# Kernel tuning notes

Hardware: AMD Instinct MI355X
Metric: run time of the kernel (lower is better)

## Reference

```python
import jax, jax.numpy as jnp
import numpy as np

UNITS = 1024
IN_DIM = 1024
B, T = 32, 2048


def setup_inputs() -> dict:
    key = jax.random.key(0)
    k1, k2, k3 = jax.random.split(key, 3)
    # glorot-uniform style scaling for weights
    lim_k = float(np.sqrt(6.0 / (IN_DIM + UNITS)))
    lim_r = float(np.sqrt(6.0 / (UNITS + UNITS)))
    x = jax.random.normal(k1, (B, T, IN_DIM), dtype=jnp.float32)
    kernel = jax.random.uniform(k2, (IN_DIM, UNITS), minval=-lim_k, maxval=lim_k, dtype=jnp.float32)
    recurrent_kernel = jax.random.uniform(k3, (UNITS, UNITS), minval=-lim_r, maxval=lim_r, dtype=jnp.float32)
    h0 = jnp.zeros((B, UNITS), dtype=jnp.float32)
    return {"x": x, "h0": h0, "kernel": kernel, "recurrent_kernel": recurrent_kernel}


def reference(x, h0, kernel, recurrent_kernel):
    # MinimalRNNCell: h_t = x_t @ W_in + h_{t-1} @ W_rec (purely linear, no activation)
    # Hoist the input projection out of the scan: one big GEMM over [B*T, IN_DIM].
    xin = jnp.einsum('btd,du->btu', x, kernel)  # [B, T, U]

    def step(h, xt):
        h_new = xt + h @ recurrent_kernel
        return h_new, None

    # scan over time axis; Keras RNN default returns the last output [B, U]
    h_last, _ = jax.lax.scan(step, h0, jnp.swapaxes(xin, 0, 1))
    return h_last
```

## Files before the change

kernel.cpp:

```cpp
#include <hip/hip_runtime.h>
#include <cstddef>
#include <cstdint>


namespace {

constexpr int BATCH = 32;
constexpr int T = 2048;
constexpr int U = 1024;
constexpr int LJ = 8;
constexpr int CJ = T / LJ;
constexpr int MJ = CJ * BATCH;

typedef _Float16 f16;
typedef _Float16 f16x4 __attribute__((ext_vector_type(4)));
typedef _Float16 f16x8 __attribute__((ext_vector_type(8)));
typedef float f32x4 __attribute__((ext_vector_type(4)));

__device__ inline void gload16(const void* g, void* l) {
    __builtin_amdgcn_global_load_lds(
        (const __attribute__((address_space(1))) unsigned int*)g,
        (__attribute__((address_space(3))) unsigned int*)l, 16, 0, 0);
}

__global__ __launch_bounds__(256)
void split_x(const float* __restrict__ x, f16* __restrict__ xh, long n4)
{
    long i = (long)blockIdx.x * 256 + threadIdx.x;
    const long stride = (long)gridDim.x * 256;
    for (; i < n4; i += stride) {
        const float4 v = *(const float4*)(x + i * 4);
        f16x4 h;
        h.x = (f16)v.x; h.y = (f16)v.y; h.z = (f16)v.z; h.w = (f16)v.w;
        *(f16x4*)(xh + i * 4) = h;
    }
}

__global__ __launch_bounds__(256)
void tsplit2(const float* __restrict__ S0, f16* __restrict__ Dh0, f16* __restrict__ Dl0,
             long dstride0, long doff0,
             const float* __restrict__ S1, f16* __restrict__ Dh1, f16* __restrict__ Dl1,
             long dstride1, long doff1)
{
    const float* S = blockIdx.z ? S1 : S0;
    f16* Dh = blockIdx.z ? Dh1 : Dh0;
    f16* Dl = blockIdx.z ? Dl1 : Dl0;
    const long dstride = blockIdx.z ? dstride1 : dstride0;
    const long doff = blockIdx.z ? doff1 : doff0;

    __shared__ float tile[32][33];
    const int t = threadIdx.x;
    const int k0 = blockIdx.x * 32;
    const int n0 = blockIdx.y * 32;
    {
        const int r = t >> 3, c4 = (t & 7) << 2;
        const float4 v = *(const float4*)(S + (size_t)(k0 + r) * U + n0 + c4);
        tile[r][c4 + 0] = v.x; tile[r][c4 + 1] = v.y;
        tile[r][c4 + 2] = v.z; tile[r][c4 + 3] = v.w;
    }
    __syncthreads();
    {
        const int c = t >> 3, r4 = (t & 7) << 2;
        float v0 = tile[r4 + 0][c], v1 = tile[r4 + 1][c],
              v2 = tile[r4 + 2][c], v3 = tile[r4 + 3][c];
        f16x4 h, lo;
        h.x = (f16)v0; lo.x = (f16)((v0 - (float)h.x) * 2048.0f);
        h.y = (f16)v1; lo.y = (f16)((v1 - (float)h.y) * 2048.0f);
        h.z = (f16)v2; lo.z = (f16)((v2 - (float)h.z) * 2048.0f);
        h.w = (f16)v3; lo.w = (f16)((v3 - (float)h.w) * 2048.0f);
        const size_t o = (size_t)(n0 + c) * dstride + doff + k0 + r4;
        *(f16x4*)(Dh + o) = h;
        *(f16x4*)(Dl + o) = lo;
    }
}

__global__ __launch_bounds__(512, 2)
void main4(const f16* __restrict__ xh, const f16* __restrict__ GhT,
           const f16* __restrict__ GlT, float* __restrict__ g0)
{
    __shared__ __align__(16) f16 LA[2][16384];
    __shared__ __align__(16) f16 LBh[2][8192];
    __shared__ __align__(16) f16 LBl[2][8192];

    const int tid  = threadIdx.x;
    const int lane = tid & 63;
    const int w    = tid >> 6;
    const int wm   = w >> 1;
    const int wn   = w & 1;
    const int r0   = blockIdx.x * 256;
    const int c0   = blockIdx.y * 128;

    const int ch  = tid & 7;
    const int rid = tid >> 3;

    size_t aof[4];
    #pragma unroll
    for (int q = 0; q < 4; ++q) {
        const int m = q * 64 + rid;
        const int arow = r0 + m;
        const size_t xbase = ((size_t)(arow & 31) * T + (size_t)(arow >> 5) * LJ) * U;
        aof[q] = xbase * 2 + (size_t)((ch ^ (m & 7)) << 4);
    }
    size_t bof[2];
    #pragma unroll
    for (int q = 0; q < 2; ++q) {
        const int c = q * 64 + rid;
        bof[q] = ((size_t)(c0 + c) << 14) + (size_t)((ch ^ (c & 7)) << 4);
    }
    const int dst = tid << 4;

    f32x4 hh[4][4], xx[4][4];
    #pragma unroll
    for (int mi = 0; mi < 4; ++mi)
        #pragma unroll
        for (int ni = 0; ni < 4; ++ni) {
            hh[mi][ni] = (f32x4){0.f, 0.f, 0.f, 0.f};
            xx[mi][ni] = (f32x4){0.f, 0.f, 0.f, 0.f};
        }

    auto stage = [&](int b, int kt) {
        const size_t kb = (size_t)kt << 7;
        #pragma unroll
        for (int q = 0; q < 4; ++q)
            gload16((const char*)xh + aof[q] + kb, (char*)&LA[b][0] + q * 8192 + dst);
        #pragma unroll
        for (int q = 0; q < 2; ++q) {
            gload16((const char*)GhT + bof[q] + kb, (char*)&LBh[b][0] + q * 8192 + dst);
            gload16((const char*)GlT + bof[q] + kb, (char*)&LBl[b][0] + q * 8192 + dst);
        }
    };

    stage(0, 0);
    __syncthreads();

    int buf = 0;
    #pragma unroll 1
    for (int kt = 0; kt < 128; ++kt) {
        if (kt + 1 < 128) stage(buf ^ 1, kt + 1);

        #pragma unroll
        for (int ks = 0; ks < 2; ++ks) {
            const int kg = ks * 4 + (lane >> 4);
            f16x8 af[4], bh[4], bl[4];
            #pragma unroll
            for (int mi = 0; mi < 4; ++mi) {
                const int rr = wm * 64 + mi * 16 + (lane & 15);
                const int byte = rr * 128 + ((kg ^ (rr & 7)) << 4);
                af[mi] = *(const f16x8*)((const char*)&LA[buf][0] + byte);
            }
            #pragma unroll
            for (int ni = 0; ni < 4; ++ni) {
                const int cc = wn * 64 + ni * 16 + (lane & 15);
                const int byte = cc * 128 + ((kg ^ (cc & 7)) << 4);
                bh[ni] = *(const f16x8*)((const char*)&LBh[buf][0] + byte);
                bl[ni] = *(const f16x8*)((const char*)&LBl[buf][0] + byte);
            }
            #pragma unroll
            for (int mi = 0; mi < 4; ++mi)
                #pragma unroll
                for (int ni = 0; ni < 4; ++ni) {
                    hh[mi][ni] = __builtin_amdgcn_mfma_f32_16x16x32_f16(af[mi], bh[ni], hh[mi][ni], 0, 0, 0);
                    xx[mi][ni] = __builtin_amdgcn_mfma_f32_16x16x32_f16(af[mi], bl[ni], xx[mi][ni], 0, 0, 0);
                }
        }
        __syncthreads();
        buf ^= 1;
    }

    #pragma unroll
    for (int mi = 0; mi < 4; ++mi)
        #pragma unroll
        for (int ni = 0; ni < 4; ++ni) {
            const int col = c0 + wn * 64 + ni * 16 + (lane & 15);
            #pragma unroll
            for (int r = 0; r < 4; ++r) {
                const int row = r0 + wm * 64 + mi * 16 + ((lane >> 4) << 2) + r;
                g0[(size_t)row * U + col] = hh[mi][ni][r] + xx[mi][ni][r] * (1.0f / 2048.0f);
            }
        }
}

struct MDesc {
    const float* A;
    const f16* BhT; const f16* BlT;
    float* C;
    f16* EhT; f16* ElT;
    long bstride, estride, eoff;
    int M, K;
    int amode;
    int cmode;
    float ascale, cscale, escale;
};

__global__ __launch_bounds__(256, 2)
void mk(MDesc d0, MDesc d1)
{
    MDesc d = blockIdx.z ? d1 : d0;
    const int r0 = blockIdx.y * 128;
    if (r0 >= d.M) return;
    const int c0 = blockIdx.x * 64;

    __shared__ __align__(16) f16 SMEM[24576];
    f16 (*LAs)[2][4096] = (f16(*)[2][4096])(&SMEM[0]);
    f16 (*LBs)[2][2048] = (f16(*)[2][2048])(&SMEM[16384]);

    const int tid = threadIdx.x;
    const int lane = tid & 63;
    const int w = tid >> 6;
    const int wm = w >> 1, wn = w & 1;

    const int arr = tid >> 1;
    const int ahalf = tid & 1;
    int arow = r0 + arr;
    if (arow >= d.M) arow = d.M - 1;
    const float* aP;
    if (d.amode == 2)
        aP = d.A + ((size_t)(((arow >> 5) << 6) + (arow & 31)) << 10);
    else
        aP = d.A + (size_t)arow * d.K;
    aP += ahalf * 16;
    int awb[2];
    #pragma unroll
    for (int j = 0; j < 2; ++j) {
        const int prow = arr >> 1;
        const int chn = 4 * (arr & 1) + 2 * ahalf + j;
        awb[j] = prow * 128 + ((chn ^ (prow & 7)) << 4);
    }

    const int bprow = tid >> 3;
    const int bslot = tid & 7;
    const int bchn  = bslot ^ (bprow & 7);
    const size_t bsrc = (size_t)(c0 + 2 * bprow + (bchn >> 2)) * (size_t)d.bstride * 2
                      + (size_t)((bchn & 3) << 4);
    const int bdst = tid * 16;

    f32x4 hh[4][2], xx[4][2];
    #pragma unroll
    for (int mi = 0; mi < 4; ++mi)
        #pragma unroll
        for (int ni = 0; ni < 2; ++ni) {
            hh[mi][ni] = (f32x4){0.f, 0.f, 0.f, 0.f};
            xx[mi][ni] = (f32x4){0.f, 0.f, 0.f, 0.f};
        }

    float4 areg[4];
    auto aload = [&](int kt) {
        const float* ap = aP + (size_t)kt * 32;
        #pragma unroll
        for (int i = 0; i < 4; ++i) areg[i] = *(const float4*)(ap + i * 4);
    };
    auto awrite = [&](int b) {
        #pragma unroll
        for (int j = 0; j < 2; ++j) {
            f16x8 h8, l8;
            #pragma unroll
            for (int e = 0; e < 2; ++e) {
                float4 v = areg[j * 2 + e];
                v.x *= d.ascale; v.y *= d.ascale; v.z *= d.ascale; v.w *= d.ascale;
                #pragma unroll
                for (int t2 = 0; t2 < 4; ++t2) {
                    const float f = (&v.x)[t2];
                    const f16 hv = (f16)f;
                    h8[e * 4 + t2] = hv;
                    l8[e * 4 + t2] = (f16)((f - (float)hv) * 2048.0f);
                }
            }
            *(f16x8*)((char*)&LAs[b][0][0] + awb[j]) = h8;
            *(f16x8*)((char*)&LAs[b][1][0] + awb[j]) = l8;
        }
    };
    auto bload = [&](int b, int kt) {
        const size_t kb = (size_t)kt << 6;
        gload16((const char*)d.BhT + bsrc + kb, (char*)&LBs[b][0][0] + bdst);
        gload16((const char*)d.BlT + bsrc + kb, (char*)&LBs[b][1][0] + bdst);
    };

    aload(0); bload(0, 0); awrite(0);
    __syncthreads();

    const int NT = d.K >> 5;
    int buf = 0;
    #pragma unroll 1
    for (int kt = 0; kt < NT; ++kt) {
        const bool more = (kt + 1 < NT);
        if (more) { aload(kt + 1); bload(buf ^ 1, kt + 1); }

        {
            const int kg = lane >> 4;
            f16x8 ah[4], al[4], bh[2], bl[2];
            #pragma unroll
            for (int mi = 0; mi < 4; ++mi) {
                const int rr = wm * 64 + mi * 16 + (lane & 15);
                const int prow = rr >> 1;
                const int chn = 4 * (rr & 1) + kg;
                const int byte = prow * 128 + ((chn ^ (prow & 7)) << 4);
                ah[mi] = *(const f16x8*)((const char*)&LAs[buf][0][0] + byte);
                al[mi] = *(const f16x8*)((const char*)&LAs[buf][1][0] + byte);
            }
            #pragma unroll
            for (int ni = 0; ni < 2; ++ni) {
                const int cc = wn * 32 + ni * 16 + (lane & 15);
                const int prow = cc >> 1;
                const int chn = 4 * (cc & 1) + kg;
                const int byte = prow * 128 + ((chn ^ (prow & 7)) << 4);
                bh[ni] = *(const f16x8*)((const char*)&LBs[buf][0][0] + byte);
                bl[ni] = *(const f16x8*)((const char*)&LBs[buf][1][0] + byte);
            }
            #pragma unroll
            for (int mi = 0; mi < 4; ++mi)
                #pragma unroll
                for (int ni = 0; ni < 2; ++ni) {
                    hh[mi][ni] = __builtin_amdgcn_mfma_f32_16x16x32_f16(ah[mi], bh[ni], hh[mi][ni], 0, 0, 0);
                    xx[mi][ni] = __builtin_amdgcn_mfma_f32_16x16x32_f16(ah[mi], bl[ni], xx[mi][ni], 0, 0, 0);
                    xx[mi][ni] = __builtin_amdgcn_mfma_f32_16x16x32_f16(al[mi], bh[ni], xx[mi][ni], 0, 0, 0);
                }
        }

        if (more) awrite(buf ^ 1);
        __syncthreads();
        buf ^= 1;
    }

    const bool emit = (d.EhT != nullptr);
    f16* Ehs = &SMEM[0];
    f16* Els = &SMEM[8192];

    #pragma unroll
    for (int mi = 0; mi < 4; ++mi) {
        #pragma unroll
        for (int ni = 0; ni < 2; ++ni) {
            const int orow = wm * 64 + mi * 16 + ((lane >> 4) << 2);
            const int colL = wn * 32 + ni * 16 + (lane & 15);
            const int col  = c0 + colL;
            float v[4];
            #pragma unroll
            for (int r = 0; r < 4; ++r)
                v[r] = (hh[mi][ni][r] + xx[mi][ni][r] * (1.0f / 2048.0f)) * d.cscale;
            if (d.C) {
                #pragma unroll
                for (int r = 0; r < 4; ++r) {
                    const int grow = r0 + orow + r;
                    if (grow < d.M) {
                        float o = v[r];
                        if (d.amode == 2) {
                            const int arow2 = (((grow >> 5) << 6) + (grow & 31)) + 32;
                            o += d.A[(size_t)arow2 * U + col];
                        }
                        float* cp = d.C + (size_t)grow * U + col;
                        if (d.cmode == 1) *cp += o; else *cp = o;
                    }
                }
            }
            if (emit) {
                f16x4 h4, l4;
                #pragma unroll
                for (int r = 0; r < 4; ++r) {
                    const float e = v[r] * d.escale;
                    h4[r] = (f16)e;
                    l4[r] = (f16)((e - (float)h4[r]) * 2048.0f);
                }
                const int blk = orow >> 3;
                const int boff = colL * 256 + ((blk ^ (colL & 15)) << 4) + (orow & 7) * 2;
                *(f16x4*)((char*)Ehs + boff) = h4;
                *(f16x4*)((char*)Els + boff) = l4;
            }
        }
    }

    if (emit) {
        __syncthreads();
        const int c  = tid & 63;
        const int b0 = (tid >> 6) * 4;
        const size_t gbase = (size_t)(c0 + c) * d.estride + d.eoff + (size_t)r0;
        #pragma unroll
        for (int i = 0; i < 4; ++i) {
            const int blk = b0 + i;
            const int off = c * 256 + ((blk ^ (c & 15)) << 4);
            *(f16x8*)(d.EhT + gbase + blk * 8) = *(const f16x8*)((char*)Ehs + off);
            *(f16x8*)(d.ElT + gbase + blk * 8) = *(const f16x8*)((char*)Els + off);
        }
    }
}

}

extern "C" void kernel_launch(void* const* d_in, const int* in_sizes, int n_in,
                              void* d_out, int out_size, void* d_ws, size_t ws_size,
                              hipStream_t stream) {
    const float* x  = (const float*)d_in[0];
    const float* h0 = (const float*)d_in[1];
    const float* W  = (const float*)d_in[2];
    const float* R  = (const float*)d_in[3];
    float* out = (float*)d_out;

    const size_t UU = (size_t)U * U;
    float* Gf  = (float*)d_ws;
    float* g0  = Gf + 4 * UU;
    float* g1  = g0 + (size_t)MJ * U;
    float* Rp2 = g1 + (size_t)(MJ / 2) * U;
    float* Rp4 = Rp2 + UU;
    float* Qa  = Rp4 + UU;
    float* Qb  = Qa + UU;
    f16* GhT = (f16*)(Qb + UU);
    f16* GlT = GhT + (size_t)U * 8192;
    f16* Tb  = GlT + (size_t)U * 8192;
    f16* Th[5]; f16* Tl[5];
    for (int i = 0; i < 5; ++i) { Th[i] = Tb + (size_t)i * 2 * UU; Tl[i] = Th[i] + UU; }
    f16* xh = Tb + 10 * UU;

    auto MD = [](const float* A, const f16* Bh, const f16* Bl, float* C,
                 f16* Eh, f16* El, long eoff, long estride, long bstride,
                 int M, int K, int amode, int cmode,
                 float as_, float cs_, float es_) {
        MDesc d;
        d.A = A; d.BhT = Bh; d.BlT = Bl; d.C = C; d.EhT = Eh; d.ElT = El;
        d.bstride = bstride; d.estride = estride; d.eoff = eoff;
        d.M = M; d.K = K; d.amode = amode; d.cmode = cmode;
        d.ascale = as_; d.cscale = cs_; d.escale = es_;
        return d;
    };
    MDesc dz = MD(nullptr, nullptr, nullptr, nullptr, nullptr, nullptr,
                  0, 0, 1024, 0, 64, 0, 0, 1.f, 1.f, 1.f);
    auto MKpair = [&](MDesc a, MDesc b) {
        int y0 = (a.M + 127) >> 7, y1 = (b.M + 127) >> 7;
        int y = y0 > y1 ? y0 : y1; if (y < 1) y = 1;
        mk<<<dim3(U / 64, (unsigned)y, 2), 256, 0, stream>>>(a, b);
    };

    split_x<<<2048, 256, 0, stream>>>(x, xh, (long)BATCH * T * U / 4);
    tsplit2<<<dim3(32, 32, 2), 256, 0, stream>>>(R, Th[0], Tl[0], 1024, 0,
                                                 W, GhT, GlT, 8192, 7 * 1024);
    hipMemcpyAsync(Gf + 3 * UU, W, UU * sizeof(float), hipMemcpyDeviceToDevice, stream);

    MKpair(MD(R,   Th[0], Tl[0], Rp2,        Th[1], Tl[1], 0,    1024, 1024, U,     U, 0, 0, 1.f, 1.f, 1.f),
           MD(W,   Th[0], Tl[0], Gf + 2*UU,  GhT,   GlT,   6144, 8192, 1024, U,     U, 0, 0, 1.f, 1.f, 1.f));
    MKpair(MD(Rp2, Th[1], Tl[1], Rp4,        Th[2], Tl[2], 0,    1024, 1024, U,     U, 0, 0, 1.f, 1.f, 1.f),
           MD(Gf + 2*UU, Th[1], Tl[1], Gf,   GhT,   GlT,   4096, 8192, 1024, 2 * U, U, 0, 0, 1.f, 1.f, 1.f));
    MKpair(MD(Rp4, Th[2], Tl[2], Qa,         Th[3], Tl[3], 0,    1024, 1024, U,     U, 0, 0, 1.f, 1.f, 1.f),
           MD(Gf,  Th[2], Tl[2], nullptr,    GhT,   GlT,   0,    8192, 1024, 4 * U, U, 0, 0, 1.f, 1.f, 1.f));

    main4<<<dim3(32, 8), 512, 0, stream>>>(xh, GhT, GlT, g0);

    MKpair(MD(h0, Th[3], Tl[3], g0, nullptr, nullptr, 0, 0, 1024, BATCH, U, 0, 1, 1.f, 1.f, 1.f), dz);

    const float aS[8] = {1.f, 1.f, 1.f, 1.f, 1.f,
                         1.f / 64.f, 1.f / 1048576.f, 7.105427357601002e-15f};
    const float cS[8] = {1.f, 1.f, 1.f, 1.f, 1.f,
                         64.f, 68719476736.f , 1.5474250491067253e26f };
    float* Qcur = Qa; float* Qnxt = Qb;
    int tcur = 3, tnxt = 4;
    float* cur = g0; float* nxt = g1;
    for (int l = 0; l < 8; ++l) {
        const int M = BATCH * ((CJ / 2) >> l);
        MDesc dc = MD(cur, Th[tcur], Tl[tcur], (l == 7) ? out : nxt,
                      nullptr, nullptr, 0, 0, 1024, M, U, 2, 0, aS[l], cS[l], 1.f);
        MDesc dq = dz;
        if (l < 7) {
            float sq_as = 1.f, sq_cs = 1.f, sq_es = 1.f;
            float* sqC = Qnxt;
            if (l == 5) { sq_es = 1.0f / 65536.0f; }
            if (l == 6) { sq_as = 1.0f / 16777216.0f; sqC = nullptr; }
            dq = MD(Qcur, Th[tcur], Tl[tcur], sqC, Th[tnxt], Tl[tnxt],
                    0, 1024, 1024, U, U, 0, 0, sq_as, sq_cs, sq_es);
        }
        MKpair(dc, dq);
        float* tq = Qcur; Qcur = Qnxt; Qnxt = tq;
        int ts = tcur; tcur = tnxt; tnxt = ts;
        float* tg = cur; cur = nxt; nxt = tg;
    }
    (void)in_sizes; (void)n_in; (void)out_size; (void)ws_size;
}
```

Before: 839.2 us.

## Pre-split GEMM A operands into fp16 hi/lo and stage via direct LDS loads

Producers now write the fp16 hi/lo split of their fp32 outputs into separate row-major buffers, alongside the transposed split they already wrote. Consumer GEMMs can then load the A operand with global_load_lds, as B already is, instead of reading fp32, scaling and splitting in registers and writing LDS. The scan schedule is also restructured: the Q-power chain is shifted one step ahead, with the first Q step paired with the h0 correction, and a third g buffer is rotated. This removes per-tile conversion ALU work and register staging from the GEMM main loop. In exchange, producers issue extra scattered fp16 stores, and the workspace holds many more split copies.

```diff
diff --git a/kernel.cpp b/kernel.cpp
--- a/kernel.cpp
+++ b/kernel.cpp
@@ -37,16 +37,22 @@
 }
 
 __global__ __launch_bounds__(256)
-void tsplit2(const float* __restrict__ S0, f16* __restrict__ Dh0, f16* __restrict__ Dl0,
-             long dstride0, long doff0,
-             const float* __restrict__ S1, f16* __restrict__ Dh1, f16* __restrict__ Dl1,
-             long dstride1, long doff1)
+void prep(const float* __restrict__ R, const float* __restrict__ W,
+          const float* __restrict__ h0,
+          f16* __restrict__ TTRh, f16* __restrict__ TTRl,
+          f16* __restrict__ Rrh, f16* __restrict__ Rrl,
+          f16* __restrict__ GhT, f16* __restrict__ GlT,
+          f16* __restrict__ Wrh, f16* __restrict__ Wrl,
+          f16* __restrict__ h0rh, f16* __restrict__ h0rl)
 {
-    const float* S = blockIdx.z ? S1 : S0;
-    f16* Dh = blockIdx.z ? Dh1 : Dh0;
-    f16* Dl = blockIdx.z ? Dl1 : Dl0;
-    const long dstride = blockIdx.z ? dstride1 : dstride0;
-    const long doff = blockIdx.z ? doff1 : doff0;
+    const int z = blockIdx.z;
+    const float* S = z ? W : R;
+    f16* Dh = z ? GhT : TTRh;
+    f16* Dl = z ? GlT : TTRl;
+    const long dstride = z ? 8192 : 1024;
+    const long doff = z ? 7168 : 0;
+    f16* Rh_ = z ? Wrh : Rrh;
+    f16* Rl_ = z ? Wrl : Rrl;
 
     __shared__ float tile[32][33];
     const int t = threadIdx.x;
@@ -57,6 +63,14 @@
         const float4 v = *(const float4*)(S + (size_t)(k0 + r) * U + n0 + c4);
         tile[r][c4 + 0] = v.x; tile[r][c4 + 1] = v.y;
         tile[r][c4 + 2] = v.z; tile[r][c4 + 3] = v.w;
+        f16x4 h, lo;
+        h.x = (f16)v.x; lo.x = (f16)((v.x - (float)h.x) * 2048.0f);
+        h.y = (f16)v.y; lo.y = (f16)((v.y - (float)h.y) * 2048.0f);
+        h.z = (f16)v.z; lo.z = (f16)((v.z - (float)h.z) * 2048.0f);
+        h.w = (f16)v.w; lo.w = (f16)((v.w - (float)h.w) * 2048.0f);
+        const size_t ro = (size_t)(k0 + r) * U + n0 + c4;
+        *(f16x4*)(Rh_ + ro) = h;
+        *(f16x4*)(Rl_ + ro) = lo;
     }
     __syncthreads();
     {
@@ -72,11 +86,24 @@
         *(f16x4*)(Dh + o) = h;
         *(f16x4*)(Dl + o) = lo;
     }
+    if (z == 1 && blockIdx.x == 0) {
+        const int r = t >> 3, c4 = (t & 7) << 2;
+        const float4 v = *(const float4*)(h0 + (size_t)r * U + n0 + c4);
+        f16x4 h, lo;
+        h.x = (f16)v.x; lo.x = (f16)((v.x - (float)h.x) * 2048.0f);
+        h.y = (f16)v.y; lo.y = (f16)((v.y - (float)h.y) * 2048.0f);
+        h.z = (f16)v.z; lo.z = (f16)((v.z - (float)h.z) * 2048.0f);
+        h.w = (f16)v.w; lo.w = (f16)((v.w - (float)h.w) * 2048.0f);
+        const size_t ro = (size_t)r * U + n0 + c4;
+        *(f16x4*)(h0rh + ro) = h;
+        *(f16x4*)(h0rl + ro) = lo;
+    }
 }
 
 __global__ __launch_bounds__(512, 2)
 void main4(const f16* __restrict__ xh, const f16* __restrict__ GhT,
-           const f16* __restrict__ GlT, float* __restrict__ g0)
+           const f16* __restrict__ GlT, float* __restrict__ g0,
+           f16* __restrict__ g0rh, f16* __restrict__ g0rl)
 {
     __shared__ __align__(16) f16 LA[2][16384];
     __shared__ __align__(16) f16 LBh[2][8192];
@@ -175,25 +202,32 @@
             #pragma unroll
             for (int r = 0; r < 4; ++r) {
                 const int row = r0 + wm * 64 + mi * 16 + ((lane >> 4) << 2) + r;
-                g0[(size_t)row * U + col] = hh[mi][ni][r] + xx[mi][ni][r] * (1.0f / 2048.0f);
+                const float val = hh[mi][ni][r] + xx[mi][ni][r] * (1.0f / 2048.0f);
+                const size_t o = (size_t)row * U + col;
+                g0[o] = val;
+                const f16 hv = (f16)val;
+                g0rh[o] = hv;
+                g0rl[o] = (f16)((val - (float)hv) * 2048.0f);
             }
         }
 }
 
 struct MDesc {
-    const float* A;
+    const f16* Ah; const f16* Al;
     const f16* BhT; const f16* BlT;
+    const float* Aadd;
     float* C;
     f16* EhT; f16* ElT;
-    long bstride, estride, eoff;
-    int M, K;
+    f16* Rh; f16* Rl;
+    long estride, eoff;
+    int M;
     int amode;
     int cmode;
-    float ascale, cscale, escale;
+    float cscale, escale, fescale;
 };
 
 __global__ __launch_bounds__(256, 2)
-void mk(MDesc d0, MDesc d1)
+void mk2(MDesc d0, MDesc d1)
 {
     MDesc d = blockIdx.z ? d1 : d0;
     const int r0 = blockIdx.y * 128;
@@ -209,28 +243,22 @@
     const int w = tid >> 6;
     const int wm = w >> 1, wn = w & 1;
 
-    const int arr = tid >> 1;
-    const int ahalf = tid & 1;
-    int arow = r0 + arr;
-    if (arow >= d.M) arow = d.M - 1;
-    const float* aP;
-    if (d.amode == 2)
-        aP = d.A + ((size_t)(((arow >> 5) << 6) + (arow & 31)) << 10);
-    else
-        aP = d.A + (size_t)arow * d.K;
-    aP += ahalf * 16;
-    int awb[2];
-    #pragma unroll
-    for (int j = 0; j < 2; ++j) {
-        const int prow = arr >> 1;
-        const int chn = 4 * (arr & 1) + 2 * ahalf + j;
-        awb[j] = prow * 128 + ((chn ^ (prow & 7)) << 4);
-    }
-
+    size_t asrc[2]; int adst[2];
+    #pragma unroll
+    for (int i = 0; i < 2; ++i) {
+        const int c = tid + 256 * i;
+        const int prow = c >> 3;
+        const int chn = (c & 7) ^ (prow & 7);
+        const int row = 2 * prow + (chn >> 2);
+        int gr = r0 + row;
+        if (gr >= d.M) gr = d.M - 1;
+        const int ar = (d.amode == 2) ? (((gr >> 5) << 6) + (gr & 31)) : gr;
+        asrc[i] = (size_t)ar * 2048 + (size_t)((chn & 3) << 4);
+        adst[i] = c * 16;
+    }
     const int bprow = tid >> 3;
-    const int bslot = tid & 7;
-    const int bchn  = bslot ^ (bprow & 7);
-    const size_t bsrc = (size_t)(c0 + 2 * bprow + (bchn >> 2)) * (size_t)d.bstride * 2
+    const int bchn = (tid & 7) ^ (bprow & 7);
+    const size_t bsrc = (size_t)(c0 + 2 * bprow + (bchn >> 2)) * 2048
                       + (size_t)((bchn & 3) << 4);
     const int bdst = tid * 16;
 
@@ -243,47 +271,24 @@
             xx[mi][ni] = (f32x4){0.f, 0.f, 0.f, 0.f};
         }
 
-    float4 areg[4];
-    auto aload = [&](int kt) {
-        const float* ap = aP + (size_t)kt * 32;
-        #pragma unroll
-        for (int i = 0; i < 4; ++i) areg[i] = *(const float4*)(ap + i * 4);
-    };
-    auto awrite = [&](int b) {
-        #pragma unroll
-        for (int j = 0; j < 2; ++j) {
-            f16x8 h8, l8;
-            #pragma unroll
-            for (int e = 0; e < 2; ++e) {
-                float4 v = areg[j * 2 + e];
-                v.x *= d.ascale; v.y *= d.ascale; v.z *= d.ascale; v.w *= d.ascale;
-                #pragma unroll
-                for (int t2 = 0; t2 < 4; ++t2) {
-                    const float f = (&v.x)[t2];
-                    const f16 hv = (f16)f;
-                    h8[e * 4 + t2] = hv;
-                    l8[e * 4 + t2] = (f16)((f - (float)hv) * 2048.0f);
-                }
-            }
-            *(f16x8*)((char*)&LAs[b][0][0] + awb[j]) = h8;
-            *(f16x8*)((char*)&LAs[b][1][0] + awb[j]) = l8;
-        }
-    };
-    auto bload = [&](int b, int kt) {
+    auto stage = [&](int b, int kt) {
         const size_t kb = (size_t)kt << 6;
+        #pragma unroll
+        for (int i = 0; i < 2; ++i) {
+            gload16((const char*)d.Ah + asrc[i] + kb, (char*)&LAs[b][0][0] + adst[i]);
+            gload16((const char*)d.Al + asrc[i] + kb, (char*)&LAs[b][1][0] + adst[i]);
+        }
         gload16((const char*)d.BhT + bsrc + kb, (char*)&LBs[b][0][0] + bdst);
         gload16((const char*)d.BlT + bsrc + kb, (char*)&LBs[b][1][0] + bdst);
     };
 
-    aload(0); bload(0, 0); awrite(0);
+    stage(0, 0);
     __syncthreads();
 
-    const int NT = d.K >> 5;
     int buf = 0;
     #pragma unroll 1
-    for (int kt = 0; kt < NT; ++kt) {
-        const bool more = (kt + 1 < NT);
-        if (more) { aload(kt + 1); bload(buf ^ 1, kt + 1); }
+    for (int kt = 0; kt < 32; ++kt) {
+        if (kt + 1 < 32) stage(buf ^ 1, kt + 1);
 
         {
             const int kg = lane >> 4;
@@ -315,13 +320,11 @@
                     xx[mi][ni] = __builtin_amdgcn_mfma_f32_16x16x32_f16(al[mi], bh[ni], xx[mi][ni], 0, 0, 0);
                 }
         }
-
-        if (more) awrite(buf ^ 1);
         __syncthreads();
         buf ^= 1;
     }
 
-    const bool emit = (d.EhT != nullptr);
+    const bool temit = (d.EhT != nullptr);
     f16* Ehs = &SMEM[0];
     f16* Els = &SMEM[8192];
 
@@ -332,30 +335,34 @@
             const int orow = wm * 64 + mi * 16 + ((lane >> 4) << 2);
             const int colL = wn * 32 + ni * 16 + (lane & 15);
             const int col  = c0 + colL;
-            float v[4];
-            #pragma unroll
-            for (int r = 0; r < 4; ++r)
-                v[r] = (hh[mi][ni][r] + xx[mi][ni][r] * (1.0f / 2048.0f)) * d.cscale;
-            if (d.C) {
-                #pragma unroll
-                for (int r = 0; r < 4; ++r) {
-                    const int grow = r0 + orow + r;
-                    if (grow < d.M) {
-                        float o = v[r];
-                        if (d.amode == 2) {
-                            const int arow2 = (((grow >> 5) << 6) + (grow & 31)) + 32;
-                            o += d.A[(size_t)arow2 * U + col];
-                        }
+            float o[4];
+            #pragma unroll
+            for (int r = 0; r < 4; ++r) {
+                o[r] = (hh[mi][ni][r] + xx[mi][ni][r] * (1.0f / 2048.0f)) * d.cscale;
+                const int grow = r0 + orow + r;
+                if (grow < d.M) {
+                    if (d.amode == 2) {
+                        const int arow2 = (((grow >> 5) << 6) + (grow & 31)) + 32;
+                        o[r] += d.Aadd[(size_t)arow2 * U + col];
+                    }
+                    if (d.C) {
                         float* cp = d.C + (size_t)grow * U + col;
-                        if (d.cmode == 1) *cp += o; else *cp = o;
+                        if (d.cmode == 1) o[r] += *cp;
+                        *cp = o[r];
+                    }
+                    if (d.Rh) {
+                        const float e = o[r] * d.fescale;
+                        const f16 hv = (f16)e;
+                        d.Rh[(size_t)grow * U + col] = hv;
+                        d.Rl[(size_t)grow * U + col] = (f16)((e - (float)hv) * 2048.0f);
                     }
                 }
             }
-            if (emit) {
+            if (temit && (r0 + orow) < d.M) {
                 f16x4 h4, l4;
                 #pragma unroll
                 for (int r = 0; r < 4; ++r) {
-                    const float e = v[r] * d.escale;
+                    const float e = o[r] * d.escale;
                     h4[r] = (f16)e;
                     l4[r] = (f16)((e - (float)h4[r]) * 2048.0f);
                 }
@@ -367,7 +374,7 @@
         }
     }
 
-    if (emit) {
+    if (temit) {
         __syncthreads();
         const int c  = tid & 63;
         const int b0 = (tid >> 6) * 4;
@@ -393,80 +400,105 @@
     const float* R  = (const float*)d_in[3];
     float* out = (float*)d_out;
 
-    const size_t UU = (size_t)U * U;
-    float* Gf  = (float*)d_ws;
-    float* g0  = Gf + 4 * UU;
-    float* g1  = g0 + (size_t)MJ * U;
-    float* Rp2 = g1 + (size_t)(MJ / 2) * U;
-    float* Rp4 = Rp2 + UU;
-    float* Qa  = Rp4 + UU;
-    float* Qb  = Qa + UU;
-    f16* GhT = (f16*)(Qb + UU);
-    f16* GlT = GhT + (size_t)U * 8192;
-    f16* Tb  = GlT + (size_t)U * 8192;
-    f16* Th[5]; f16* Tl[5];
-    for (int i = 0; i < 5; ++i) { Th[i] = Tb + (size_t)i * 2 * UU; Tl[i] = Th[i] + UU; }
-    f16* xh = Tb + 10 * UU;
-
-    auto MD = [](const float* A, const f16* Bh, const f16* Bl, float* C,
-                 f16* Eh, f16* El, long eoff, long estride, long bstride,
-                 int M, int K, int amode, int cmode,
-                 float as_, float cs_, float es_) {
+    const size_t M1 = (size_t)1024 * 1024;
+    float* g0 = (float*)d_ws;
+    float* gA = g0 + 8 * M1;
+    float* gB = gA + 4 * M1;
+    f16* fp = (f16*)(gB + 4 * M1);
+    auto take = [&](size_t n) { f16* r = fp; fp += n; return r; };
+    f16* xh   = take(64 * M1);
+    f16* GhT  = take(8 * M1);
+    f16* GlT  = take(8 * M1);
+    f16* Tqh[8]; f16* Tql[8];
+    for (int l = 0; l < 8; ++l) { Tqh[l] = take(M1); Tql[l] = take(M1); }
+    f16* Qrh[7]; f16* Qrl[7];
+    for (int l = 0; l < 7; ++l) { Qrh[l] = take(M1); Qrl[l] = take(M1); }
+    f16* Gfrh = take(4 * M1); f16* Gfrl = take(4 * M1);
+    f16* h0rh = take(32 * 1024); f16* h0rl = take(32 * 1024);
+    f16* g0rh = take(8 * M1); f16* g0rl = take(8 * M1);
+    f16* gArh = take(4 * M1); f16* gArl = take(4 * M1);
+    f16* gBrh = take(4 * M1); f16* gBrl = take(4 * M1);
+    f16* TTRh = Tqh[3]; f16* TTRl = Tql[3];
+    f16* TT1h = Tqh[1]; f16* TT1l = Tql[1];
+    f16* TT2h = Tqh[2]; f16* TT2l = Tql[2];
+    f16* Rrh  = Qrh[3]; f16* Rrl  = Qrl[3];
+    f16* R2rh = Qrh[1]; f16* R2rl = Qrl[1];
+    f16* R4rh = Qrh[2]; f16* R4rl = Qrl[2];
+
+    auto MD2 = [](const f16* Ah, const f16* Al, const f16* Bh, const f16* Bl,
+                  const float* Aadd, float* C, f16* Eh, f16* El, long eoff, long estride,
+                  f16* Rh, f16* Rl, int M, int amode, int cmode,
+                  float cs, float es, float fs) {
         MDesc d;
-        d.A = A; d.BhT = Bh; d.BlT = Bl; d.C = C; d.EhT = Eh; d.ElT = El;
-        d.bstride = bstride; d.estride = estride; d.eoff = eoff;
-        d.M = M; d.K = K; d.amode = amode; d.cmode = cmode;
-        d.ascale = as_; d.cscale = cs_; d.escale = es_;
+        d.Ah = Ah; d.Al = Al; d.BhT = Bh; d.BlT = Bl; d.Aadd = Aadd; d.C = C;
+        d.EhT = Eh; d.ElT = El; d.Rh = Rh; d.Rl = Rl;
+        d.estride = estride; d.eoff = eoff; d.M = M; d.amode = amode; d.cmode = cmode;
+        d.cscale = cs; d.escale = es; d.fescale = fs;
         return d;
     };
-    MDesc dz = MD(nullptr, nullptr, nullptr, nullptr, nullptr, nullptr,
-                  0, 0, 1024, 0, 64, 0, 0, 1.f, 1.f, 1.f);
-    auto MKpair = [&](MDesc a, MDesc b) {
+    MDesc dz = MD2(nullptr, nullptr, nullptr, nullptr, nullptr, nullptr,
+                   nullptr, nullptr, 0, 1024, nullptr, nullptr, 0, 0, 0, 1.f, 1.f, 1.f);
+    auto PAIR = [&](MDesc a, MDesc b) {
         int y0 = (a.M + 127) >> 7, y1 = (b.M + 127) >> 7;
         int y = y0 > y1 ? y0 : y1; if (y < 1) y = 1;
-        mk<<<dim3(U / 64, (unsigned)y, 2), 256, 0, stream>>>(a, b);
+        mk2<<<dim3(16, (unsigned)y, 2), 256, 0, stream>>>(a, b);
     };
 
     split_x<<<2048, 256, 0, stream>>>(x, xh, (long)BATCH * T * U / 4);
-    tsplit2<<<dim3(32, 32, 2), 256, 0, stream>>>(R, Th[0], Tl[0], 1024, 0,
-                                                 W, GhT, GlT, 8192, 7 * 1024);
-    hipMemcpyAsync(Gf + 3 * UU, W, UU * sizeof(float), hipMemcpyDeviceToDevice, stream);
-
-    MKpair(MD(R,   Th[0], Tl[0], Rp2,        Th[1], Tl[1], 0,    1024, 1024, U,     U, 0, 0, 1.f, 1.f, 1.f),
-           MD(W,   Th[0], Tl[0], Gf + 2*UU,  GhT,   GlT,   6144, 8192, 1024, U,     U, 0, 0, 1.f, 1.f, 1.f));
-    MKpair(MD(Rp2, Th[1], Tl[1], Rp4,        Th[2], Tl[2], 0,    1024, 1024, U,     U, 0, 0, 1.f, 1.f, 1.f),
-           MD(Gf + 2*UU, Th[1], Tl[1], Gf,   GhT,   GlT,   4096, 8192, 1024, 2 * U, U, 0, 0, 1.f, 1.f, 1.f));
-    MKpair(MD(Rp4, Th[2], Tl[2], Qa,         Th[3], Tl[3], 0,    1024, 1024, U,     U, 0, 0, 1.f, 1.f, 1.f),
-           MD(Gf,  Th[2], Tl[2], nullptr,    GhT,   GlT,   0,    8192, 1024, 4 * U, U, 0, 0, 1.f, 1.f, 1.f));
-
-    main4<<<dim3(32, 8), 512, 0, stream>>>(xh, GhT, GlT, g0);
-
-    MKpair(MD(h0, Th[3], Tl[3], g0, nullptr, nullptr, 0, 0, 1024, BATCH, U, 0, 1, 1.f, 1.f, 1.f), dz);
-
-    const float aS[8] = {1.f, 1.f, 1.f, 1.f, 1.f,
-                         1.f / 64.f, 1.f / 1048576.f, 7.105427357601002e-15f};
+    prep<<<dim3(32, 32, 2), 256, 0, stream>>>(R, W, h0, TTRh, TTRl, Rrh, Rrl,
+                                              GhT, GlT,
+                                              Gfrh + 3 * M1, Gfrl + 3 * M1,
+                                              h0rh, h0rl);
+
+    PAIR(MD2(Rrh, Rrl, TTRh, TTRl, nullptr, nullptr, TT1h, TT1l, 0, 1024,
+             R2rh, R2rl, U, 0, 0, 1.f, 1.f, 1.f),
+         MD2(Gfrh + 3 * M1, Gfrl + 3 * M1, TTRh, TTRl, nullptr, nullptr,
+             GhT, GlT, 6144, 8192, Gfrh + 2 * M1, Gfrl + 2 * M1, U, 0, 0, 1.f, 1.f, 1.f));
+    PAIR(MD2(R2rh, R2rl, TT1h, TT1l, nullptr, nullptr, TT2h, TT2l, 0, 1024,
+             R4rh, R4rl, U, 0, 0, 1.f, 1.f, 1.f),
+         MD2(Gfrh + 2 * M1, Gfrl + 2 * M1, TT1h, TT1l, nullptr, nullptr,
+             GhT, GlT, 4096, 8192, Gfrh, Gfrl, 2 * U, 0, 0, 1.f, 1.f, 1.f));
+    PAIR(MD2(R4rh, R4rl, TT2h, TT2l, nullptr, nullptr, Tqh[0], Tql[0], 0, 1024,
+             Qrh[0], Qrl[0], U, 0, 0, 1.f, 1.f, 1.f),
+         MD2(Gfrh, Gfrl, TT2h, TT2l, nullptr, nullptr,
+             GhT, GlT, 0, 8192, nullptr, nullptr, 4 * U, 0, 0, 1.f, 1.f, 1.f));
+
+    main4<<<dim3(32, 8), 512, 0, stream>>>(xh, GhT, GlT, g0, g0rh, g0rl);
+
+    PAIR(MD2(h0rh, h0rl, Tqh[0], Tql[0], nullptr, g0, nullptr, nullptr, 0, 1024,
+             g0rh, g0rl, BATCH, 0, 1, 1.f, 1.f, 1.f),
+         MD2(Qrh[0], Qrl[0], Tqh[0], Tql[0], nullptr, nullptr, Tqh[1], Tql[1], 0, 1024,
+             Qrh[1], Qrl[1], U, 0, 0, 1.f, 1.f, 1.f));
+
+    const float aS[9] = {1.f, 1.f, 1.f, 1.f, 1.f,
+                         0.015625f, 9.5367431640625e-07f, 7.105427357601002e-15f, 0.f};
     const float cS[8] = {1.f, 1.f, 1.f, 1.f, 1.f,
-                         64.f, 68719476736.f , 1.5474250491067253e26f };
-    float* Qcur = Qa; float* Qnxt = Qb;
-    int tcur = 3, tnxt = 4;
-    float* cur = g0; float* nxt = g1;
+                         64.f, 68719476736.f, 1.5474250491067253e26f};
+    float* gcur = g0; f16* gcrh = g0rh; f16* gcrl = g0rl;
+    float* gnxt = gA; f16* gnrh = gArh; f16* gnrl = gArl;
+    float* gprv = gB; f16* gprh = gBrh; f16* gprl = gBrl;
     for (int l = 0; l < 8; ++l) {
         const int M = BATCH * ((CJ / 2) >> l);
-        MDesc dc = MD(cur, Th[tcur], Tl[tcur], (l == 7) ? out : nxt,
-                      nullptr, nullptr, 0, 0, 1024, M, U, 2, 0, aS[l], cS[l], 1.f);
+        MDesc dc = MD2(gcrh, gcrl, Tqh[l], Tql[l], gcur, (l == 7) ? out : gnxt,
+                       nullptr, nullptr, 0, 1024,
+                       (l < 7) ? gnrh : nullptr, (l < 7) ? gnrl : nullptr,
+                       M, 2, 0, cS[l], 1.f, aS[l + 1]);
         MDesc dq = dz;
-        if (l < 7) {
-            float sq_as = 1.f, sq_cs = 1.f, sq_es = 1.f;
-            float* sqC = Qnxt;
-            if (l == 5) { sq_es = 1.0f / 65536.0f; }
-            if (l == 6) { sq_as = 1.0f / 16777216.0f; sqC = nullptr; }
-            dq = MD(Qcur, Th[tcur], Tl[tcur], sqC, Th[tnxt], Tl[tnxt],
-                    0, 1024, 1024, U, U, 0, 0, sq_as, sq_cs, sq_es);
-        }
-        MKpair(dc, dq);
-        float* tq = Qcur; Qcur = Qnxt; Qnxt = tq;
-        int ts = tcur; tcur = tnxt; tnxt = ts;
-        float* tg = cur; cur = nxt; nxt = tg;
+        if (l < 6) {
+            const int s = l + 1;
+            const float fe = (s == 5) ? 5.960464477539063e-08f : 1.f;
+            const float te = (s == 5) ? 1.52587890625e-05f : 1.f;
+            f16* reh = (s + 1 <= 6) ? Qrh[s + 1] : nullptr;
+            f16* rel = (s + 1 <= 6) ? Qrl[s + 1] : nullptr;
+            dq = MD2(Qrh[s], Qrl[s], Tqh[s], Tql[s], nullptr, nullptr,
+                     Tqh[s + 1], Tql[s + 1], 0, 1024, reh, rel, U, 0, 0, 1.f, te, fe);
+        }
+        PAIR(dc, dq);
+        float* tf = gprv; gprv = gcur; gcur = gnxt; gnxt = tf;
+        f16* th = gprh; f16* tl = gprl;
+        gprh = gcrh; gprl = gcrl;
+        gcrh = gnrh; gcrl = gnrl;
+        gnrh = th;   gnrl = tl;
     }
     (void)in_sizes; (void)n_in; (void)out_size; (void)ws_size;
 }
```

Result: faster. 802.4 us (-4.4%).
